# Kernel optimization log

Hardware: AMD Instinct MI355X
Metric: run time of the kernel (lower is better)

Reference implementation:

```python
import jax, jax.numpy as jnp
import numpy as np

B, S, D = 4, 2048, 1024
H, HD = 16, 64            # num heads, head dim (H*HD == D)
FF = 4096                  # llama intermediate size
EPS = 1e-6
THETA = 10000.0


def rms_norm(x, w):
    v = jnp.mean(jnp.square(x), axis=-1, keepdims=True)
    return x * jax.lax.rsqrt(v + EPS) * w


def apply_rope(x, pos):
    # x: [B,H,S,HD]; HF llama rotate_half convention
    inv = 1.0 / (THETA ** (jnp.arange(0, HD, 2, dtype=jnp.float32) / HD))  # [HD/2]
    ang = pos[:, None].astype(jnp.float32) * inv[None, :]                   # [S,HD/2]
    cos = jnp.concatenate([jnp.cos(ang), jnp.cos(ang)], -1)[None, None]     # [1,1,S,HD]
    sin = jnp.concatenate([jnp.sin(ang), jnp.sin(ang)], -1)[None, None]
    x1, x2 = jnp.split(x, 2, axis=-1)
    return x * cos + jnp.concatenate([-x2, x1], axis=-1) * sin


def setup_inputs() -> dict:
    key = jax.random.key(0)
    ks = jax.random.split(key, 12)
    p = lambda k, shp: (0.02 * jax.random.normal(k, shp, dtype=jnp.float32))
    return {
        "chunk_hidden_states": jax.random.normal(ks[0], (B, S, D), dtype=jnp.float32),
        "Wq": p(ks[1], (D, D)),
        "Wk": p(ks[2], (D, D)),
        "Wv": p(ks[3], (D, D)),
        "Wo": p(ks[4], (D, D)),
        "ln1_w": jnp.ones((D,), dtype=jnp.float32),
        "ln2_w": jnp.ones((D,), dtype=jnp.float32),
        "Wgate": p(ks[5], (FF, D)),
        "Wup": p(ks[6], (FF, D)),
        "Wdown": p(ks[7], (D, FF)),
        "W_out": p(ks[8], (1024, D)),
        "b_out": jnp.zeros((1024,), dtype=jnp.float32),
    }


def reference(chunk_hidden_states, Wq, Wk, Wv, Wo, ln1_w, ln2_w,
              Wgate, Wup, Wdown, W_out, b_out):
    x = chunk_hidden_states                      # [B,S,D]
    pos = jnp.arange(S)

    # --- self attention block ---
    h = rms_norm(x, ln1_w)
    q = (h @ Wq.T).reshape(B, S, H, HD).transpose(0, 2, 1, 3)  # [B,H,S,HD]
    k = (h @ Wk.T).reshape(B, S, H, HD).transpose(0, 2, 1, 3)
    v = (h @ Wv.T).reshape(B, S, H, HD).transpose(0, 2, 1, 3)
    q = apply_rope(q, pos)
    k = apply_rope(k, pos)
    # attention_mask is None when the layer is called directly -> full (non-causal) attention
    scores = jnp.einsum("bhqd,bhkd->bhqk", q, k) / jnp.sqrt(jnp.float32(HD))
    attn = jax.nn.softmax(scores, axis=-1)
    ctx = jnp.einsum("bhqk,bhkd->bhqd", attn, v)             # [B,H,S,HD]
    ctx = ctx.transpose(0, 2, 1, 3).reshape(B, S, D)
    x = x + ctx @ Wo.T

    # --- MLP block (SwiGLU) ---
    h2 = rms_norm(x, ln2_w)
    mlp = (jax.nn.silu(h2 @ Wgate.T) * (h2 @ Wup.T)) @ Wdown.T
    x = x + mlp

    # --- output head ---
    logits = x @ W_out.T + b_out                 # [B,S,1024]
    return logits.reshape(-1, 8, 1024)
```

## Files before the change

### kernel.cpp

```cpp
#include <hip/hip_runtime.h>

#define TB 4
#define TS 2048
#define TD 1024
#define TH 16
#define THD 64
#define TFF 4096
#define TTOK (TB*TS)

typedef unsigned int  uint32;
typedef unsigned short u16;
typedef short s8v __attribute__((ext_vector_type(8)));
typedef short s4bf __attribute__((ext_vector_type(4)));
typedef float f4v __attribute__((ext_vector_type(4)));

#define BF16_MAGIC 0x3f803f80u

__device__ __forceinline__ u16 f2bf(float f){
    uint32 u = __float_as_uint(f);
    u += 0x7fffu + ((u >> 16) & 1u);
    return (u16)(u >> 16);
}
__device__ __forceinline__ float bf2f(u16 h){
    return __uint_as_float(((uint32)h) << 16);
}
__device__ __forceinline__ void gload_lds16(const void* g, void* l){
    __builtin_amdgcn_global_load_lds(
        (const __attribute__((address_space(1))) unsigned int*)g,
        (__attribute__((address_space(3))) unsigned int*)l,
        16, 0, 0);
}
__device__ __forceinline__ void bar(){
    asm volatile("" ::: "memory");
    __builtin_amdgcn_s_barrier();
    asm volatile("" ::: "memory");
}
#define WAITVM4() asm volatile("s_waitcnt vmcnt(4)" ::: "memory")
#define WAITVM2() asm volatile("s_waitcnt vmcnt(2)" ::: "memory")
#define WAITVM0() asm volatile("s_waitcnt vmcnt(0)" ::: "memory")

struct CvtDesc { const void* src; void* dst; int n; int mode; };
struct CvtArgs { CvtDesc d[13]; };

__global__ __launch_bounds__(256)
void cvt_all(CvtArgs a, const uint32* __restrict__ flag){
    const bool isbf = (*flag == BF16_MAGIC);
    CvtDesc dd = a.d[blockIdx.y];
    if (dd.mode == 2){
        float* cosT = (float*)dd.dst;
        float* sinT = cosT + TS*32;
        for (int i = blockIdx.x*256 + threadIdx.x; i < dd.n; i += 256*gridDim.x){
            int s = i >> 5, f = i & 31;
            double inv = pow(10000.0, -(double)f/32.0);
            double ang = (double)s * inv;
            cosT[i] = (float)cos(ang);
            sinT[i] = (float)sin(ang);
        }
        return;
    }
    int n4 = dd.n >> 2;
    if (dd.mode == 1){
        float* dst = (float*)dd.dst;
        for (int i = blockIdx.x*256 + threadIdx.x; i < n4; i += 256*gridDim.x){
            float4 v;
            if (isbf){
                ushort4 u = ((const ushort4*)dd.src)[i];
                v = make_float4(bf2f(u.x), bf2f(u.y), bf2f(u.z), bf2f(u.w));
            } else v = ((const float4*)dd.src)[i];
            ((float4*)dst)[i] = v;
        }
        return;
    }
    for (int i = blockIdx.x*256 + threadIdx.x; i < n4; i += 256*gridDim.x){
        ushort4 o;
        if (isbf) o = ((const ushort4*)dd.src)[i];
        else {
            float4 v = ((const float4*)dd.src)[i];
            o.x=f2bf(v.x); o.y=f2bf(v.y); o.z=f2bf(v.z); o.w=f2bf(v.w);
        }
        size_t di = i;
        if (dd.mode >= 3){
            int row = i >> 8, c4 = i & 255;
            int drow = ((row >> 6) << 7) + (row & 63) + ((dd.mode == 4) ? 64 : 0);
            di = (size_t)drow*256 + c4;
        }
        ((ushort4*)dd.dst)[di] = o;
    }
}

__global__ __launch_bounds__(256)
void rmsnorm_k(const float* __restrict__ x, const float* __restrict__ w, u16* __restrict__ out){
    int row = blockIdx.x, tid = threadIdx.x;
    float4 xv = ((const float4*)(x + (size_t)row*TD))[tid];
    float s = xv.x*xv.x + xv.y*xv.y + xv.z*xv.z + xv.w*xv.w;
    #pragma unroll
    for (int off = 32; off > 0; off >>= 1) s += __shfl_xor(s, off);
    __shared__ float red[4];
    if ((tid & 63) == 0) red[tid >> 6] = s;
    __syncthreads();
    float tot = red[0]+red[1]+red[2]+red[3];
    float rs = rsqrtf(tot * (1.0f/TD) + 1e-6f);
    float4 wv = ((const float4*)w)[tid];
    ushort4 o;
    o.x = f2bf(xv.x*rs*wv.x); o.y = f2bf(xv.y*rs*wv.y);
    o.z = f2bf(xv.z*rs*wv.z); o.w = f2bf(xv.w*rs*wv.w);
    ((ushort4*)(out + (size_t)row*TD))[tid] = o;
}

enum { EPI_ADDF32 = 1, EPI_OUT = 3, EPI_QKVROPE = 4, EPI_ADDBF16 = 5, EPI_GATEUP = 6 };

template<int EPI>
__global__ __launch_bounds__(256)
void gemm_bt(const u16* __restrict__ A, int lda,
             const u16* __restrict__ W, int ldw,
             int K,
             void* __restrict__ outp, int ldo,
             const float* __restrict__ bias,
             const uint32* __restrict__ flag,
             u16* __restrict__ q_out, u16* __restrict__ k_out, u16* __restrict__ vt_out,
             const float* __restrict__ cosT, const float* __restrict__ sinT,
             const float* __restrict__ resid)
{
    __shared__ __align__(16) u16 SMEM[2*128*64];
    u16* As = SMEM;
    u16* Bs = SMEM + 128*64;
    const int tid  = threadIdx.x;
    const int wave = tid >> 6;
    const int lane = tid & 63;
    const int nbx = gridDim.x;
    const int lin = blockIdx.y * nbx + blockIdx.x;
    const int swz = (lin & 7) * ((nbx * gridDim.y) >> 3) + (lin >> 3);
    const int tm = (swz / nbx) * 128;
    const int tn = (swz % nbx) * 128;
    const int wm = (wave >> 1) * 64;
    const int wn = (wave &  1) * 64;

    f4v acc[4][4] = {};

    const int srow8 = lane >> 3;
    const int ch    = lane & 7;
    const int lrow  = lane & 15;
    const int lq    = lane >> 4;

    const u16* Ag = A + (size_t)(tm + wave*32 + srow8)*lda + ((ch ^ srow8) << 3);
    const u16* Wg = W + (size_t)(tn + wave*32 + srow8)*ldw + ((ch ^ srow8) << 3);

    for (int k0 = 0; k0 < K; k0 += 64){
        __syncthreads();
        #pragma unroll
        for (int i8 = 0; i8 < 4; i8++){
            gload_lds16(Ag + (size_t)(i8*8)*lda + k0, As + (wave*32 + i8*8)*64);
            gload_lds16(Wg + (size_t)(i8*8)*ldw + k0, Bs + (wave*32 + i8*8)*64);
        }
        __syncthreads();

        #pragma unroll
        for (int kk = 0; kk < 2; kk++){
            s8v a[4], b[4];
            #pragma unroll
            for (int i = 0; i < 4; i++){
                int row = wm + i*16 + lrow;
                a[i] = *(const s8v*)(As + row*64 + (((kk*4 + lq) ^ (lrow & 7)) << 3));
            }
            #pragma unroll
            for (int j = 0; j < 4; j++){
                int row = wn + j*16 + lrow;
                b[j] = *(const s8v*)(Bs + row*64 + (((kk*4 + lq) ^ (lrow & 7)) << 3));
            }
            #pragma unroll
            for (int i = 0; i < 4; i++)
                #pragma unroll
                for (int j = 0; j < 4; j++)
                    acc[i][j] = __builtin_amdgcn_mfma_f32_16x16x32_bf16(a[i], b[j], acc[i][j], 0, 0, 0);
        }
    }

    if constexpr (EPI == EPI_QKVROPE){
        const int ncol0 = tn + wn;
        if (ncol0 < 2048){
            u16* dst = (ncol0 < 1024) ? q_out : k_out;
            const int cbase = ncol0 & 1023;
            #pragma unroll
            for (int i = 0; i < 4; i++){
                #pragma unroll
                for (int r = 0; r < 4; r++){
                    int row = tm + wm + i*16 + lq*4 + r;
                    int s = row & (TS-1);
                    #pragma unroll
                    for (int j = 0; j < 2; j++){
                        int d = j*16 + lrow;
                        float c  = cosT[s*32 + d];
                        float sn = sinT[s*32 + d];
                        float x1 = acc[i][j][r], x2 = acc[i][j+2][r];
                        dst[(size_t)row*TD + cbase + d]      = f2bf(x1*c - x2*sn);
                        dst[(size_t)row*TD + cbase + d + 32] = f2bf(x2*c + x1*sn);
                    }
                }
            }
        } else {
            #pragma unroll
            for (int i = 0; i < 4; i++)
                #pragma unroll
                for (int j = 0; j < 4; j++)
                    #pragma unroll
                    for (int r = 0; r < 4; r++){
                        int row = tm + wm + i*16 + lq*4 + r;
                        int col = ncol0 - 2048 + j*16 + lrow;
                        int bb = row >> 11, s = row & (TS-1);
                        int hh = col >> 6, hd = col & 63;
                        vt_out[((size_t)(bb*TH + hh)*THD + hd)*TS + s] = f2bf(acc[i][j][r]);
                    }
        }
        return;
    }

    bool obf = false;
    if (EPI == EPI_OUT) obf = (*flag == BF16_MAGIC);
    #pragma unroll
    for (int i = 0; i < 4; i++){
        #pragma unroll
        for (int j = 0; j < 4; j++){
            #pragma unroll
            for (int r = 0; r < 4; r++){
                int row = tm + wm + i*16 + lq*4 + r;
                int col = tn + wn + j*16 + lrow;
                size_t idx = (size_t)row*ldo + col;
                float val = acc[i][j][r];
                if constexpr (EPI == EPI_ADDF32){
                    float* o = (float*)outp;
                    o[idx] += val;
                } else if constexpr (EPI == EPI_ADDBF16){
                    ((u16*)outp)[idx] = f2bf(resid[idx] + val);
                } else {
                    float v2 = val + bias[col];
                    if (obf) ((u16*)outp)[idx] = f2bf(v2);
                    else     ((float*)outp)[idx] = v2;
                }
            }
        }
    }
}

template<int EPI>
__global__ __launch_bounds__(512, 2)
void gemm256(const u16* __restrict__ A, int lda,
             const u16* __restrict__ W, int ldw,
             int K,
             void* __restrict__ outp, int ldo,
             const float* __restrict__ resid)
{
    __shared__ __align__(16) u16 SM[2][2*256*64];
    const int tid  = threadIdx.x;
    const int wave = tid >> 6;
    const int lane = tid & 63;
    const int wm = wave >> 2;
    const int wn = wave & 3;
    const int lrow = lane & 15;
    const int lq   = lane >> 4;
    const int srow8 = lane >> 3;
    const int ch    = lane & 7;

    const int nbx = gridDim.x;
    const int lin = blockIdx.y * nbx + blockIdx.x;
    const int swz = (lin & 7) * ((nbx * gridDim.y) >> 3) + (lin >> 3);
    const int tm = (swz / nbx) * 256;
    const int tn = (swz % nbx) * 256;

    const int NT = K >> 6;

    const u16* Ag = A + (size_t)(tm + wave*8 + srow8)*lda + ((ch ^ srow8) << 3);
    const u16* Wg = W + (size_t)(tn + wave*8 + srow8)*ldw + ((ch ^ srow8) << 3);

    f4v acc[2][4][2][2] = {};
    s8v a[2][4];
    s8v b[2][2][2];

    auto stageA = [&](int bufi, int g, int t){
        size_t k0 = (size_t)t * 64;
        #pragma unroll
        for (int r = 0; r < 2; r++)
            gload_lds16(Ag + (size_t)(g*128 + r*64)*lda + k0,
                        &SM[bufi][(g*128 + r*64 + wave*8)*64]);
    };
    auto stageB = [&](int bufi, int h, int t){
        size_t k0 = (size_t)t * 64;
        #pragma unroll
        for (int r = 0; r < 2; r++)
            gload_lds16(Wg + (size_t)(h*128 + r*64)*ldw + k0,
                        &SM[bufi][256*64 + (h*128 + r*64 + wave*8)*64]);
    };
    auto ldA = [&](int bufi, int g){
        #pragma unroll
        for (int kk = 0; kk < 2; kk++)
            #pragma unroll
            for (int i = 0; i < 4; i++){
                int row = g*128 + wm*64 + i*16 + lrow;
                a[kk][i] = *(const s8v*)(&SM[bufi][row*64 + (((kk*4 + lq) ^ (lrow & 7)) << 3)]);
            }
    };
    auto ldB = [&](int bufi, int h){
        #pragma unroll
        for (int kk = 0; kk < 2; kk++)
            #pragma unroll
            for (int j = 0; j < 2; j++){
                int row = h*128 + wn*32 + j*16 + lrow;
                b[h][kk][j] = *(const s8v*)(&SM[bufi][256*64 + row*64 + (((kk*4 + lq) ^ (lrow & 7)) << 3)]);
            }
    };
    auto mmac = [&](int g, int h){
        __builtin_amdgcn_s_setprio(1);
        #pragma unroll
        for (int kk = 0; kk < 2; kk++)
            #pragma unroll
            for (int i = 0; i < 4; i++)
                #pragma unroll
                for (int j = 0; j < 2; j++)
                    acc[g][i][h][j] = __builtin_amdgcn_mfma_f32_16x16x32_bf16(
                        a[kk][i], b[h][kk][j], acc[g][i][h][j], 0, 0, 0);
        __builtin_amdgcn_s_setprio(0);
    };

    stageA(0,0,0); stageB(0,0,0); stageB(0,1,0); stageA(0,1,0);
    WAITVM4(); bar();

    for (int t = 0; t < NT-1; t++){
        const int buf = t & 1, nb = buf ^ 1;
        ldA(buf,0); ldB(buf,0);
        stageA(nb,0,t+1);
        bar();
        mmac(0,0);
        WAITVM4(); bar();
        ldB(buf,1);
        stageB(nb,0,t+1);
        bar();
        mmac(0,1);
        WAITVM4(); bar();
        ldA(buf,1);
        stageB(nb,1,t+1);
        bar();
        mmac(1,0);
        bar();
        stageA(nb,1,t+1);
        bar();
        mmac(1,1);
        WAITVM4(); bar();
    }
    {
        const int buf = (NT-1) & 1;
        ldA(buf,0); ldB(buf,0);
        bar();
        mmac(0,0);
        WAITVM2(); bar();
        ldB(buf,1);
        bar();
        mmac(0,1);
        WAITVM0(); bar();
        ldA(buf,1);
        bar();
        mmac(1,0);
        bar();
        mmac(1,1);
    }

    if constexpr (EPI == EPI_GATEUP){
        bar();
        float* X = (float*)&SM[0][0];
        const int uw = wm*2 + (wn & 1);
        if (wn >= 2){
            #pragma unroll
            for (int g = 0; g < 2; g++)
            #pragma unroll
            for (int i = 0; i < 4; i++)
            #pragma unroll
            for (int h = 0; h < 2; h++)
            #pragma unroll
            for (int j = 0; j < 2; j++)
            #pragma unroll
            for (int r = 0; r < 4; r++)
                X[uw*8192 + (g*64 + i*16 + lq*4 + r)*64
                          + ((h*32 + j*16 + lrow) ^ (lq << 3))] = acc[g][i][h][j][r];
        }
        bar();
        if (wn < 2){
            u16* o = (u16*)outp;
            #pragma unroll
            for (int g = 0; g < 2; g++)
            #pragma unroll
            for (int i = 0; i < 4; i++)
            #pragma unroll
            for (int h = 0; h < 2; h++)
            #pragma unroll
            for (int j = 0; j < 2; j++)
            #pragma unroll
            for (int r = 0; r < 4; r++){
                float gv = acc[g][i][h][j][r];
                float uv = X[uw*8192 + (g*64 + i*16 + lq*4 + r)*64
                                     + ((h*32 + j*16 + lrow) ^ (lq << 3))];
                float mres = (gv / (1.0f + __expf(-gv))) * uv;
                int row = tm + g*128 + wm*64 + i*16 + lq*4 + r;
                int ff  = (tn >> 1) + h*64 + wn*32 + j*16 + lrow;
                o[(size_t)row*TFF + ff] = f2bf(mres);
            }
        }
        return;
    }

    if constexpr (EPI == EPI_ADDBF16){
        u16* o = (u16*)outp;
        #pragma unroll
        for (int g = 0; g < 2; g++)
        #pragma unroll
        for (int i = 0; i < 4; i++)
        #pragma unroll
        for (int h = 0; h < 2; h++)
        #pragma unroll
        for (int j = 0; j < 2; j++)
        #pragma unroll
        for (int r = 0; r < 4; r++){
            int row = tm + g*128 + wm*64 + i*16 + lq*4 + r;
            int col = tn + h*128 + wn*32 + j*16 + lrow;
            size_t idx = (size_t)row*ldo + col;
            o[idx] = f2bf(resid[idx] + acc[g][i][h][j][r]);
        }
        return;
    }
}

__global__ __launch_bounds__(256, 2)
void flash_attn_mfma(const u16* __restrict__ qg, const u16* __restrict__ kg,
                     const u16* __restrict__ vt, u16* __restrict__ ctx)
{
    __shared__ u16 Qs[128*64];
    __shared__ u16 Ks[64*64];
    __shared__ u16 VT2[8*64*8];
    const int tid  = threadIdx.x;
    const int wave = tid >> 6;
    const int lane = tid & 63;
    const int qd   = lane >> 4;
    const int mm   = lane & 15;
    const int lin = blockIdx.y * 16 + blockIdx.x;
    const int swz = (lin & 7) * 128 + (lin >> 3);
    const int b  = swz >> 8, h = (swz >> 4) & 15;
    const int q0 = (swz & 15) * 128;
    const size_t tok0 = (size_t)b * TS;
    const u16* vtb = vt + (size_t)(b*TH + h)*THD*TS;
    const int rl = lane >> 3, ch = lane & 7;

    #pragma unroll
    for (int i = 0; i < 4; i++){
        int row = wave*32 + i*8 + rl;
        const u16* gp = qg + (tok0 + q0 + row)*TD + h*THD + ((ch ^ (row & 7)) << 3);
        gload_lds16(gp, Qs + (wave*32 + i*8)*64);
    }
    __syncthreads();

    s8v qf[2][2];
    #pragma unroll
    for (int ct = 0; ct < 2; ct++){
        int row = wave*32 + ct*16 + mm;
        #pragma unroll
        for (int hs = 0; hs < 2; hs++)
            qf[ct][hs] = *(const s8v*)(Qs + row*64 + (((hs*4 + qd) ^ (row & 7)) << 3));
    }

    f4v acc[2][4] = {};
    float mrun[2] = {-3.0e38f, -3.0e38f};
    float lrun[2] = {0.0f, 0.0f};
    const float SC2 = 0.18033688011112042f;

    for (int kt = 0; kt < TS/64; kt++){
        __syncthreads();
        #pragma unroll
        for (int i = 0; i < 2; i++){
            int row = wave*16 + i*8 + rl;
            const u16* gp = kg + (tok0 + kt*64 + row)*TD + h*THD + ((ch ^ (row & 7)) << 3);
            gload_lds16(gp, Ks + (wave*16 + i*8)*64);
        }
        #pragma unroll
        for (int ii = 0; ii < 2; ii++){
            int kb = wave*2 + ii;
            const u16* gp = vtb + (size_t)lane*TS + kt*64 + kb*8;
            gload_lds16(gp, VT2 + kb*64*8);
        }
        __syncthreads();

        f4v sc[4][2] = {};
        #pragma unroll
        for (int rt = 0; rt < 4; rt++){
            int row = rt*16 + mm;
            #pragma unroll
            for (int hs = 0; hs < 2; hs++){
                s8v kf = *(const s8v*)(Ks + row*64 + (((hs*4 + qd) ^ (row & 7)) << 3));
                #pragma unroll
                for (int ct = 0; ct < 2; ct++)
                    sc[rt][ct] = __builtin_amdgcn_mfma_f32_16x16x32_bf16(kf, qf[ct][hs], sc[rt][ct], 0, 0, 0);
            }
        }
        union VU { s4bf h[2]; s8v v; };
        VU vf8[2][4];
        #pragma unroll
        for (int t = 0; t < 2; t++){
            int kbA = 4*t + (qd >> 1);
            #pragma unroll
            for (int n = 0; n < 4; n++){
                const u16* base = VT2 + ((16*n + mm)*8) + ((qd & 1) * 4);
                vf8[t][n].h[0] = *(const s4bf*)(base + kbA*512);
                vf8[t][n].h[1] = *(const s4bf*)(base + (kbA+2)*512);
            }
        }

        #pragma unroll
        for (int ct = 0; ct < 2; ct++){
            float mx = sc[0][ct][0];
            #pragma unroll
            for (int rt = 0; rt < 4; rt++)
                #pragma unroll
                for (int r = 0; r < 4; r++)
                    mx = fmaxf(mx, sc[rt][ct][r]);
            mx = fmaxf(mx, __shfl_xor(mx, 16));
            mx = fmaxf(mx, __shfl_xor(mx, 32));
            float mn = fmaxf(mrun[ct], mx * SC2);
            float alpha = __builtin_amdgcn_exp2f(mrun[ct] - mn);
            mrun[ct] = mn;
            float ls = 0.0f;
            uint32 pk[4][2];
            #pragma unroll
            for (int rt = 0; rt < 4; rt++){
                float p0 = __builtin_amdgcn_exp2f(fmaf(sc[rt][ct][0], SC2, -mn));
                float p1 = __builtin_amdgcn_exp2f(fmaf(sc[rt][ct][1], SC2, -mn));
                float p2 = __builtin_amdgcn_exp2f(fmaf(sc[rt][ct][2], SC2, -mn));
                float p3 = __builtin_amdgcn_exp2f(fmaf(sc[rt][ct][3], SC2, -mn));
                ls += (p0 + p1) + (p2 + p3);
                pk[rt][0] = (__float_as_uint(p0) >> 16) | (__float_as_uint(p1) & 0xFFFF0000u);
                pk[rt][1] = (__float_as_uint(p2) >> 16) | (__float_as_uint(p3) & 0xFFFF0000u);
            }
            ls += __shfl_xor(ls, 16);
            ls += __shfl_xor(ls, 32);
            lrun[ct] = lrun[ct]*alpha + ls;
            #pragma unroll
            for (int r = 0; r < 4; r++){
                float ar = __shfl(alpha, (lane & 48) + qd*4 + r);
                #pragma unroll
                for (int n = 0; n < 4; n++)
                    acc[ct][n][r] *= ar;
            }
            #pragma unroll
            for (int t = 0; t < 2; t++){
                union { uint32 u[4]; s8v s; } pu;
                pu.u[0] = pk[2*t][0];   pu.u[1] = pk[2*t][1];
                pu.u[2] = pk[2*t+1][0]; pu.u[3] = pk[2*t+1][1];
                #pragma unroll
                for (int n = 0; n < 4; n++)
                    acc[ct][n] = __builtin_amdgcn_mfma_f32_16x16x32_bf16(pu.s, vf8[t][n].v, acc[ct][n], 0, 0, 0);
            }
        }
    }
    #pragma unroll
    for (int ct = 0; ct < 2; ct++){
        float rli = 1.0f / lrun[ct];
        #pragma unroll
        for (int r = 0; r < 4; r++){
            float ir = __shfl(rli, (lane & 48) + qd*4 + r);
            int row = q0 + wave*32 + ct*16 + qd*4 + r;
            u16* op = ctx + (tok0 + row)*TD + h*THD + mm;
            #pragma unroll
            for (int n = 0; n < 4; n++)
                op[16*n] = f2bf(acc[ct][n][r] * ir);
        }
    }
}

extern "C" void kernel_launch(void* const* d_in, const int* in_sizes, int n_in,
                              void* d_out, int out_size, void* d_ws, size_t ws_size,
                              hipStream_t stream)
{
    const uint32* flag = (const uint32*)d_in[5];
    char* ws = (char*)d_ws;
    size_t off = 0;
    auto alloc = [&](size_t bytes) -> void* {
        void* p = ws + off;
        off += (bytes + 255) & ~(size_t)255;
        return p;
    };
    float* xf   = (float*)alloc((size_t)TTOK*TD*4);
    u16*   hbf  = (u16*)  alloc((size_t)TTOK*TD*2);
    u16*   qb   = (u16*)  alloc((size_t)TTOK*TD*2);
    u16*   kb   = (u16*)  alloc((size_t)TTOK*TD*2);
    u16*   cb   = (u16*)  alloc((size_t)TTOK*TD*2);
    u16*   vt   = (u16*)  alloc((size_t)TTOK*TD*2);
    u16*   wqkv = (u16*)  alloc((size_t)3*TD*TD*2);
    u16*   wo   = (u16*)  alloc((size_t)TD*TD*2);
    u16*   wfu  = (u16*)  alloc((size_t)2*TFF*TD*2);
    u16*   wd   = (u16*)  alloc((size_t)TD*TFF*2);
    u16*   wou  = (u16*)  alloc((size_t)TD*TD*2);
    float* ln1  = (float*)alloc(TD*4);
    float* ln2  = (float*)alloc(TD*4);
    float* bo   = (float*)alloc(TD*4);
    float* cosT = (float*)alloc((size_t)TS*32*4*2);
    float* sinT = cosT + TS*32;
    u16*   mbuf = qb;
    (void)ws_size; (void)in_sizes; (void)n_in; (void)out_size;

    CvtArgs ca;
    ca.d[0]  = { d_in[0],  xf,            TTOK*TD, 1 };
    ca.d[1]  = { d_in[1],  wqkv,          TD*TD,   0 };
    ca.d[2]  = { d_in[2],  wqkv + (size_t)TD*TD,   TD*TD, 0 };
    ca.d[3]  = { d_in[3],  wqkv + (size_t)2*TD*TD, TD*TD, 0 };
    ca.d[4]  = { d_in[4],  wo,            TD*TD,   0 };
    ca.d[5]  = { d_in[7],  wfu,           TFF*TD,  3 };
    ca.d[6]  = { d_in[8],  wfu,           TFF*TD,  4 };
    ca.d[7]  = { d_in[9],  wd,            TD*TFF,  0 };
    ca.d[8]  = { d_in[10], wou,           TD*TD,   0 };
    ca.d[9]  = { d_in[5],  ln1,           TD,      1 };
    ca.d[10] = { d_in[6],  ln2,           TD,      1 };
    ca.d[11] = { d_in[11], bo,            TD,      1 };
    ca.d[12] = { nullptr,  cosT,          TS*32,   2 };
    cvt_all<<<dim3(256,13),256,0,stream>>>(ca, flag);

    rmsnorm_k<<<TTOK,256,0,stream>>>(xf, ln1, hbf);
    gemm_bt<EPI_QKVROPE><<<dim3(24, TTOK/128),256,0,stream>>>(
        hbf, TD, wqkv, TD, TD, nullptr, 0, nullptr, nullptr,
        qb, kb, vt, cosT, sinT, nullptr);
    flash_attn_mfma<<<dim3(TS/128, TB*TH),256,0,stream>>>(qb, kb, vt, cb);
    gemm_bt<EPI_ADDF32><<<dim3(TD/128, TTOK/128),256,0,stream>>>(
        cb, TD, wo, TD, TD, xf, TD, nullptr, nullptr,
        nullptr, nullptr, nullptr, nullptr, nullptr, nullptr);

    rmsnorm_k<<<TTOK,256,0,stream>>>(xf, ln2, hbf);
    gemm256<EPI_GATEUP><<<dim3(2*TFF/256, TTOK/256),512,0,stream>>>(
        hbf, TD, wfu, TD, TD, mbuf, TFF, nullptr);
    gemm256<EPI_ADDBF16><<<dim3(TD/256, TTOK/256),512,0,stream>>>(
        mbuf, TFF, wd, TFF, TFF, hbf, TD, xf);

    gemm_bt<EPI_OUT><<<dim3(TD/128, TTOK/128),256,0,stream>>>(
        hbf, TD, wou, TD, TD, d_out, TD, bo, flag,
        nullptr, nullptr, nullptr, nullptr, nullptr, nullptr);
}
```

Baseline: 701.2 us.

## Deepen gemm256 prefetch to two tiles ahead and route down-proj through gemm_bt

The 256-tile GEMM main loop now prefetches tiles t+2 into the buffer just consumed, so each global load has two iterations to land instead of one. The vmcnt waits are adjusted to match, and two peeled tail iterations drain the pipeline. Separately, the down-projection GEMM is switched from the 256x256 kernel (128 blocks) to the 128x128 gemm_bt kernel (512 blocks), which gives more blocks to fill the CUs. The deeper prefetch is sensitive to exact vmcnt counts and buffer reuse ordering, and gemm_bt must already support the EPI_ADDBF16 epilogue with the residual pointer in its last argument.

```diff
diff --git a/kernel.cpp b/kernel.cpp
--- a/kernel.cpp
+++ b/kernel.cpp
@@ -35,9 +35,7 @@
     __builtin_amdgcn_s_barrier();
     asm volatile("" ::: "memory");
 }
-#define WAITVM4() asm volatile("s_waitcnt vmcnt(4)" ::: "memory")
-#define WAITVM2() asm volatile("s_waitcnt vmcnt(2)" ::: "memory")
-#define WAITVM0() asm volatile("s_waitcnt vmcnt(0)" ::: "memory")
+#define WAITVM(N) asm volatile("s_waitcnt vmcnt(" #N ")" ::: "memory")
 
 struct CvtDesc { const void* src; void* dst; int n; int mode; };
 struct CvtArgs { CvtDesc d[13]; };
@@ -320,41 +318,62 @@
         __builtin_amdgcn_s_setprio(0);
     };
 
-    stageA(0,0,0); stageB(0,0,0); stageB(0,1,0); stageA(0,1,0);
-    WAITVM4(); bar();
-
-    for (int t = 0; t < NT-1; t++){
-        const int buf = t & 1, nb = buf ^ 1;
+    stageA(0,0,0); stageB(0,0,0);
+    stageB(0,1,0);
+    stageA(0,1,0);
+    stageA(1,0,1); stageB(1,0,1);
+    stageB(1,1,1);
+    stageA(1,1,1);
+    WAITVM(12); bar();
+
+    for (int t = 0; t < NT-2; t++){
+        const int buf = t & 1;
         ldA(buf,0); ldB(buf,0);
-        stageA(nb,0,t+1);
         bar();
         mmac(0,0);
-        WAITVM4(); bar();
+        WAITVM(10); bar();
         ldB(buf,1);
-        stageB(nb,0,t+1);
+        stageA(buf,0,t+2); stageB(buf,0,t+2);
         bar();
         mmac(0,1);
-        WAITVM4(); bar();
+        WAITVM(12); bar();
         ldA(buf,1);
-        stageB(nb,1,t+1);
+        stageB(buf,1,t+2);
         bar();
         mmac(1,0);
         bar();
-        stageA(nb,1,t+1);
+        stageA(buf,1,t+2);
         bar();
         mmac(1,1);
-        WAITVM4(); bar();
+        WAITVM(12); bar();
+    }
+    {
+        const int buf = (NT-2) & 1;
+        ldA(buf,0); ldB(buf,0);
+        bar();
+        mmac(0,0);
+        WAITVM(10); bar();
+        ldB(buf,1);
+        bar();
+        mmac(0,1);
+        WAITVM(8); bar();
+        ldA(buf,1);
+        bar();
+        mmac(1,0);
+        bar();
+        mmac(1,1);
+        WAITVM(4); bar();
     }
     {
         const int buf = (NT-1) & 1;
         ldA(buf,0); ldB(buf,0);
         bar();
         mmac(0,0);
-        WAITVM2(); bar();
+        WAITVM(2); bar();
         ldB(buf,1);
         bar();
         mmac(0,1);
-        WAITVM0(); bar();
+        WAITVM(0); bar();
         ldA(buf,1);
         bar();
         mmac(1,0);
@@ -629,8 +648,9 @@
     rmsnorm_k<<<TTOK,256,0,stream>>>(xf, ln2, hbf);
     gemm256<EPI_GATEUP><<<dim3(2*TFF/256, TTOK/256),512,0,stream>>>(
         hbf, TD, wfu, TD, TD, mbuf, TFF, nullptr);
-    gemm256<EPI_ADDBF16><<<dim3(TD/256, TTOK/256),512,0,stream>>>(
-        mbuf, TFF, wd, TFF, TFF, hbf, TD, xf);
+    gemm_bt<EPI_ADDBF16><<<dim3(TD/128, TTOK/128),256,0,stream>>>(
+        mbuf, TFF, wd, TFF, TFF, hbf, TD, nullptr, nullptr,
+        nullptr, nullptr, nullptr, nullptr, nullptr, xf);
 
     gemm_bt<EPI_OUT><<<dim3(TD/128, TTOK/128),256,0,stream>>>(
         hbf, TD, wou, TD, TD, d_out, TD, bo, flag,
```

Measured after the change: 675.7 us. -3.6%, faster.

## Deepen gemm256 prefetch pipeline and route down-projection through gemm_bt

Applied to the files above, without the earlier changes.

Reworks the gemm256 main loop to unroll by two k-tiles with statically indexed buffers. Staging of the next tile's sub-blocks is interleaved more finely, which loosens the per-step vmcnt waits and removes a barrier-bound stall pattern. Separately, the down-projection GEMM (K=4096, N=1024) is moved from the 256x256 kernel with 32 workgroups' worth of columns to the 128x128 gemm_bt kernel. That gives four times as many workgroups for better CU occupancy, at the cost of less reuse per tile. The unrolled loop assumes NT is even, and correctness depends on the buffer and stage ordering.

```diff
diff --git a/kernel.cpp b/kernel.cpp
--- a/kernel.cpp
+++ b/kernel.cpp
@@ -35,9 +35,7 @@
     __builtin_amdgcn_s_barrier();
     asm volatile("" ::: "memory");
 }
-#define WAITVM4() asm volatile("s_waitcnt vmcnt(4)" ::: "memory")
-#define WAITVM2() asm volatile("s_waitcnt vmcnt(2)" ::: "memory")
-#define WAITVM0() asm volatile("s_waitcnt vmcnt(0)" ::: "memory")
+#define WAITVM(N) asm volatile("s_waitcnt vmcnt(" #N ")" ::: "memory")
 
 struct CvtDesc { const void* src; void* dst; int n; int mode; };
 struct CvtArgs { CvtDesc d[13]; };
@@ -321,44 +319,51 @@
     };
 
     stageA(0,0,0); stageB(0,0,0); stageB(0,1,0); stageA(0,1,0);
-    WAITVM4(); bar();
-
-    for (int t = 0; t < NT-1; t++){
-        const int buf = t & 1, nb = buf ^ 1;
-        ldA(buf,0); ldB(buf,0);
-        stageA(nb,0,t+1);
-        bar();
-        mmac(0,0);
-        WAITVM4(); bar();
-        ldB(buf,1);
-        stageB(nb,0,t+1);
-        bar();
-        mmac(0,1);
-        WAITVM4(); bar();
-        ldA(buf,1);
-        stageB(nb,1,t+1);
-        bar();
-        mmac(1,0);
-        bar();
-        stageA(nb,1,t+1);
-        bar();
-        mmac(1,1);
-        WAITVM4(); bar();
+    stageA(1,0,1); stageB(1,0,1); stageB(1,1,1);
+    WAITVM(6); bar();
+
+    for (int t = 0; t < NT-2; t += 2){
+        ldA(0,0); ldB(0,0);
+        stageA(1,1,t+1);
+        bar(); mmac(0,0); bar();
+        ldB(0,1);
+        stageA(0,0,t+2);
+        bar(); mmac(0,1); bar();
+        ldA(0,1);
+        stageB(0,0,t+2);
+        bar(); mmac(1,0); bar();
+        stageB(0,1,t+2);
+        WAITVM(6);
+        bar(); mmac(1,1); bar();
+        ldA(1,0); ldB(1,0);
+        stageA(0,1,t+2);
+        bar(); mmac(0,0); bar();
+        ldB(1,1);
+        stageA(1,0,t+3);
+        bar(); mmac(0,1); bar();
+        ldA(1,1);
+        stageB(1,0,t+3);
+        bar(); mmac(1,0); bar();
+        stageB(1,1,t+3);
+        WAITVM(6);
+        bar(); mmac(1,1); bar();
     }
     {
-        const int buf = (NT-1) & 1;
-        ldA(buf,0); ldB(buf,0);
-        bar();
-        mmac(0,0);
-        WAITVM2(); bar();
-        ldB(buf,1);
-        bar();
-        mmac(0,1);
-        WAITVM0(); bar();
-        ldA(buf,1);
-        bar();
-        mmac(1,0);
-        bar();
+        ldA(0,0); ldB(0,0);
+        stageA(1,1,NT-1);
+        bar(); mmac(0,0); bar();
+        ldB(0,1);
+        bar(); mmac(0,1); bar();
+        ldA(0,1);
+        bar(); mmac(1,0); bar();
+        WAITVM(0);
+        bar(); mmac(1,1); bar();
+        ldA(1,0); ldB(1,0);
+        bar(); mmac(0,0); bar();
+        ldB(1,1);
+        bar(); mmac(0,1); bar();
+        ldA(1,1);
+        bar(); mmac(1,0); bar();
         mmac(1,1);
     }
 
@@ -629,8 +634,9 @@
     rmsnorm_k<<<TTOK,256,0,stream>>>(xf, ln2, hbf);
     gemm256<EPI_GATEUP><<<dim3(2*TFF/256, TTOK/256),512,0,stream>>>(
         hbf, TD, wfu, TD, TD, mbuf, TFF, nullptr);
-    gemm256<EPI_ADDBF16><<<dim3(TD/256, TTOK/256),512,0,stream>>>(
-        mbuf, TFF, wd, TFF, TFF, hbf, TD, xf);
+    gemm_bt<EPI_ADDBF16><<<dim3(TD/128, TTOK/128),256,0,stream>>>(
+        mbuf, TFF, wd, TFF, TFF, hbf, TD, nullptr, nullptr,
+        nullptr, nullptr, nullptr, nullptr, nullptr, xf);
 
     gemm_bt<EPI_OUT><<<dim3(TD/128, TTOK/128),256,0,stream>>>(
         hbf, TD, wou, TD, TD, d_out, TD, bo, flag,
```

Measured after the change: 702.6 us. About the same (+0.2%).
